# Performance work log

Hardware: AMD Instinct MI355X
Metric: run time of the kernel (lower is better)

## Reference

```python
import jax, jax.numpy as jnp
import numpy as np

IN_CH = 12
STEP = 4
UPLAG = 2048
HIDDEN = 1024
OUTPUT = 256
BATCH = 2048
FEAT = UPLAG // STEP  # per-channel conv output length


def setup_inputs() -> dict:
    key = jax.random.key(0)
    ks = jax.random.split(key, 7)
    s = 1.0 / np.sqrt(STEP)
    x = jax.random.normal(ks[0], (BATCH, IN_CH, UPLAG), dtype=jnp.float32)
    # per-channel Conv1d(1,1,step,step) weights/biases, stacked: [C, step], [C]
    W1 = jax.random.uniform(ks[1], (IN_CH, STEP), jnp.float32, -s, s)
    b1 = jax.random.uniform(ks[2], (IN_CH,), jnp.float32, -s, s)
    d_in = IN_CH * FEAT
    s2 = 1.0 / np.sqrt(d_in)
    W2 = jax.random.uniform(ks[3], (d_in, HIDDEN), jnp.float32, -s2, s2)
    b2 = jax.random.uniform(ks[4], (HIDDEN,), jnp.float32, -s2, s2)
    s3 = 1.0 / np.sqrt(HIDDEN)
    W3 = jax.random.uniform(ks[5], (HIDDEN, OUTPUT), jnp.float32, -s3, s3)
    b3 = jax.random.uniform(ks[6], (OUTPUT,), jnp.float32, -s3, s3)
    return {"x": x, "W1": W1, "b1": b1, "W2": W2, "b2": b2, "W3": W3, "b3": b3}


def reference(x, W1, b1, W2, b2, W3, b3):
    B, C, L = x.shape
    # Non-overlapping patch reduction equivalent to Conv1d(1,1,step,step) per channel:
    # view [B, C, F, step], contract step dim against per-channel kernel.
    xp = x.reshape(B, C, L // STEP, STEP)
    conv = jnp.einsum('bcfk,ck->bcf', xp, W1) + b1[None, :, None]  # [B, C, F]
    flat = conv.reshape(B, C * (L // STEP))  # concat order: channel-major, matches torch.cat
    h = jax.nn.relu(flat @ W2 + b2)
    out = h @ W3 + b3
    return out.reshape(B, 1, -1)
```

## Files before the change

kernel.cpp:

```cpp
#include <hip/hip_runtime.h>
#include <hip/hip_bf16.h>

#define BATCH   2048
#define IN_CH   12
#define UPLAG   2048
#define STEP    4
#define FEAT    512
#define DIN     6144
#define HIDDEN  1024
#define OUTPUT  256

typedef __bf16 bf16x8 __attribute__((ext_vector_type(8)));
typedef float  f32x4  __attribute__((ext_vector_type(4)));

__device__ __forceinline__ unsigned short f2bf(float f) {
  unsigned int u = __builtin_bit_cast(unsigned int, f);
  unsigned int r = (u + 0x7fffu + ((u >> 16) & 1u)) >> 16;
  return (unsigned short)r;
}

__device__ __forceinline__ void async_copy16(const unsigned short* g, unsigned short* l) {
  __builtin_amdgcn_global_load_lds(
      (const __attribute__((address_space(1))) unsigned int*)g,
      (__attribute__((address_space(3))) unsigned int*)l, 16, 0, 0);
}

__global__ __launch_bounds__(256) void conv_cast_kernel(
    const float* __restrict__ x, const float* __restrict__ W1,
    const float* __restrict__ b1, unsigned short* __restrict__ out)
{
  int gid = blockIdx.x * 256 + threadIdx.x;
  const int total = BATCH * DIN;
  if (gid >= total) return;
  int cf = gid % DIN;
  int c  = cf >> 9;
  float4 xv = ((const float4*)x)[gid];
  float4 wv = ((const float4*)W1)[c];
  float v = xv.x * wv.x + xv.y * wv.y + xv.z * wv.z + xv.w * wv.w + b1[c];
  out[gid] = f2bf(v);
}

__global__ __launch_bounds__(256) void transpose_cast(
    const float* __restrict__ in, unsigned short* __restrict__ out,
    int R, int Ncol)
{
  __shared__ float tile[32][33];
  int bx = blockIdx.x * 32;
  int by = blockIdx.y * 32;
  int tx = threadIdx.x, ty = threadIdx.y;
  #pragma unroll
  for (int i = 0; i < 32; i += 8)
    tile[ty + i][tx] = in[(size_t)(by + ty + i) * Ncol + bx + tx];
  __syncthreads();
  #pragma unroll
  for (int i = 0; i < 32; i += 8)
    out[(size_t)(bx + ty + i) * R + by + tx] = f2bf(tile[tx][ty + i]);
}

#define G1_BM 128
#define G1_BN 128
#define G1_BK 32
#define SPLITK 6

__global__ __launch_bounds__(256, 2) void gemm1_kernel(
    const unsigned short* __restrict__ A,
    const unsigned short* __restrict__ BT,
    float* __restrict__ Cp,
    int M, int N, int K)
{
  __shared__ unsigned short As[G1_BM * G1_BK];
  __shared__ unsigned short Bs[G1_BN * G1_BK];
  const int t    = threadIdx.x;
  const int lane = t & 63;
  const int wave = t >> 6;
  const int m0 = blockIdx.y * G1_BM;
  const int n0 = blockIdx.x * G1_BN;
  const int Ks = K / SPLITK;
  const int kbeg = blockIdx.z * Ks;

  const int wm = (wave >> 1) * 64;
  const int wn = (wave & 1) * 64;
  const int lm = lane & 15;
  const int lk = (lane >> 4) * 8;

  f32x4 acc[4][4];
  #pragma unroll
  for (int i = 0; i < 4; i++)
    #pragma unroll
    for (int j = 0; j < 4; j++) {
      f32x4 z = {0.f, 0.f, 0.f, 0.f};
      acc[i][j] = z;
    }

  const unsigned short* Ag = A  + (size_t)m0 * K + kbeg;
  const unsigned short* Bg = BT + (size_t)n0 * K + kbeg;

  for (int kk = 0; kk < Ks; kk += G1_BK) {
    #pragma unroll
    for (int r = 0; r < 2; ++r) {
      int chunk = r * 256 + t;
      int row = chunk >> 2;
      int kc  = (chunk & 3) * 8;
      async_copy16(Ag + (size_t)row * K + kk + kc, As + chunk * 8);
    }
    #pragma unroll
    for (int r = 0; r < 2; ++r) {
      int chunk = r * 256 + t;
      int row = chunk >> 2;
      int kc  = (chunk & 3) * 8;
      async_copy16(Bg + (size_t)row * K + kk + kc, Bs + chunk * 8);
    }
    __syncthreads();

    bf16x8 af[4], bfr[4];
    #pragma unroll
    for (int i = 0; i < 4; i++)
      af[i] = *(const bf16x8*)(As + (wm + i * 16 + lm) * G1_BK + lk);
    #pragma unroll
    for (int j = 0; j < 4; j++)
      bfr[j] = *(const bf16x8*)(Bs + (wn + j * 16 + lm) * G1_BK + lk);
    #pragma unroll
    for (int i = 0; i < 4; i++)
      #pragma unroll
      for (int j = 0; j < 4; j++)
        acc[i][j] = __builtin_amdgcn_mfma_f32_16x16x32_bf16(af[i], bfr[j], acc[i][j], 0, 0, 0);
    __syncthreads();
  }

  float* Co = Cp + (size_t)blockIdx.z * M * N;
  const int rbase = (lane >> 4) * 4;
  #pragma unroll
  for (int i = 0; i < 4; i++)
    #pragma unroll
    for (int j = 0; j < 4; j++) {
      int col = n0 + wn + j * 16 + lm;
      #pragma unroll
      for (int r = 0; r < 4; r++) {
        int row = m0 + wm + i * 16 + rbase + r;
        Co[(size_t)row * N + col] = acc[i][j][r];
      }
    }
}

__global__ __launch_bounds__(256) void reduce_bias_relu(
    const float* __restrict__ Cp, const float* __restrict__ b2,
    unsigned short* __restrict__ H)
{
  const int MN = BATCH * HIDDEN;
  int i4 = blockIdx.x * 256 + threadIdx.x;
  if (i4 >= MN / 4) return;
  float4 s = ((const float4*)Cp)[i4];
  #pragma unroll
  for (int p = 1; p < SPLITK; ++p) {
    float4 a = ((const float4*)(Cp + (size_t)p * MN))[i4];
    s.x += a.x; s.y += a.y; s.z += a.z; s.w += a.w;
  }
  int col = (i4 * 4) & (HIDDEN - 1);
  float4 bb = *(const float4*)(b2 + col);
  ushort4 o;
  o.x = f2bf(fmaxf(s.x + bb.x, 0.f));
  o.y = f2bf(fmaxf(s.y + bb.y, 0.f));
  o.z = f2bf(fmaxf(s.z + bb.z, 0.f));
  o.w = f2bf(fmaxf(s.w + bb.w, 0.f));
  ((ushort4*)H)[i4] = o;
}

#define SPLITK2 4

__global__ __launch_bounds__(256, 2) void gemm2_kernel(
    const unsigned short* __restrict__ A,
    const unsigned short* __restrict__ BT,
    float* __restrict__ Cp)
{
  const int M = BATCH, N = OUTPUT, K = HIDDEN;
  __shared__ unsigned short As[64 * 32];
  __shared__ unsigned short Bs[64 * 32];
  const int t    = threadIdx.x;
  const int lane = t & 63;
  const int wave = t >> 6;
  const int m0 = blockIdx.y * 64;
  const int n0 = blockIdx.x * 64;
  const int Ks = K / SPLITK2;
  const int kbeg = blockIdx.z * Ks;
  const int wm = (wave >> 1) * 32;
  const int wn = (wave & 1) * 32;
  const int lm = lane & 15;
  const int lk = (lane >> 4) * 8;
  const int row = t >> 2;
  const int kc  = (t & 3) * 8;

  f32x4 acc[2][2];
  #pragma unroll
  for (int i = 0; i < 2; i++)
    #pragma unroll
    for (int j = 0; j < 2; j++) {
      f32x4 z = {0.f, 0.f, 0.f, 0.f};
      acc[i][j] = z;
    }

  const unsigned short* Ag = A  + (size_t)m0 * K + kbeg;
  const unsigned short* Bg = BT + (size_t)n0 * K + kbeg;

  for (int kk = 0; kk < Ks; kk += 32) {
    async_copy16(Ag + (size_t)row * K + kk + kc, As + t * 8);
    async_copy16(Bg + (size_t)row * K + kk + kc, Bs + t * 8);
    __syncthreads();
    bf16x8 af[2], bfr[2];
    #pragma unroll
    for (int i = 0; i < 2; i++)
      af[i] = *(const bf16x8*)(As + (wm + i * 16 + lm) * 32 + lk);
    #pragma unroll
    for (int j = 0; j < 2; j++)
      bfr[j] = *(const bf16x8*)(Bs + (wn + j * 16 + lm) * 32 + lk);
    #pragma unroll
    for (int i = 0; i < 2; i++)
      #pragma unroll
      for (int j = 0; j < 2; j++)
        acc[i][j] = __builtin_amdgcn_mfma_f32_16x16x32_bf16(af[i], bfr[j], acc[i][j], 0, 0, 0);
    __syncthreads();
  }

  float* Co = Cp + (size_t)blockIdx.z * M * N;
  const int rbase = (lane >> 4) * 4;
  #pragma unroll
  for (int i = 0; i < 2; i++)
    #pragma unroll
    for (int j = 0; j < 2; j++) {
      int col = n0 + wn + j * 16 + lm;
      #pragma unroll
      for (int r = 0; r < 4; r++) {
        int row_o = m0 + wm + i * 16 + rbase + r;
        Co[(size_t)row_o * N + col] = acc[i][j][r];
      }
    }
}

__global__ __launch_bounds__(256) void reduce2_bias(
    const float* __restrict__ Cp, const float* __restrict__ b3,
    float* __restrict__ out)
{
  const int MN = BATCH * OUTPUT;
  int i4 = blockIdx.x * 256 + threadIdx.x;
  if (i4 >= MN / 4) return;
  float4 s = ((const float4*)Cp)[i4];
  #pragma unroll
  for (int p = 1; p < SPLITK2; ++p) {
    float4 a = ((const float4*)(Cp + (size_t)p * MN))[i4];
    s.x += a.x; s.y += a.y; s.z += a.z; s.w += a.w;
  }
  int col = (i4 * 4) & (OUTPUT - 1);
  float4 bb = *(const float4*)(b3 + col);
  float4 o = {s.x + bb.x, s.y + bb.y, s.z + bb.z, s.w + bb.w};
  ((float4*)out)[i4] = o;
}

extern "C" void kernel_launch(void* const* d_in, const int* in_sizes, int n_in,
                              void* d_out, int out_size, void* d_ws, size_t ws_size,
                              hipStream_t stream)
{
  const float* x  = (const float*)d_in[0];
  const float* W1 = (const float*)d_in[1];
  const float* b1 = (const float*)d_in[2];
  const float* W2 = (const float*)d_in[3];
  const float* b2 = (const float*)d_in[4];
  const float* W3 = (const float*)d_in[5];
  const float* b3 = (const float*)d_in[6];
  float* out = (float*)d_out;

  char* ws = (char*)d_ws;
  unsigned short* flatA = (unsigned short*)ws; ws += (size_t)BATCH * DIN * 2;
  unsigned short* W2T   = (unsigned short*)ws; ws += (size_t)HIDDEN * DIN * 2;
  unsigned short* W3T   = (unsigned short*)ws; ws += (size_t)OUTPUT * HIDDEN * 2;
  float*          Cpart = (float*)ws;          ws += (size_t)SPLITK * BATCH * HIDDEN * 4;
  unsigned short* H     = (unsigned short*)ws; ws += (size_t)BATCH * HIDDEN * 2;
  float*          Cp2   = (float*)ws;          ws += (size_t)SPLITK2 * BATCH * OUTPUT * 4;

  conv_cast_kernel<<<(BATCH * DIN) / 256, 256, 0, stream>>>(x, W1, b1, flatA);
  transpose_cast<<<dim3(HIDDEN / 32, DIN / 32), dim3(32, 8), 0, stream>>>(W2, W2T, DIN, HIDDEN);
  transpose_cast<<<dim3(OUTPUT / 32, HIDDEN / 32), dim3(32, 8), 0, stream>>>(W3, W3T, HIDDEN, OUTPUT);
  gemm1_kernel<<<dim3(HIDDEN / G1_BN, BATCH / G1_BM, SPLITK), 256, 0, stream>>>(
      flatA, W2T, Cpart, BATCH, HIDDEN, DIN);
  reduce_bias_relu<<<(BATCH * HIDDEN / 4) / 256, 256, 0, stream>>>(Cpart, b2, H);
  gemm2_kernel<<<dim3(OUTPUT / 64, BATCH / 64, SPLITK2), 256, 0, stream>>>(H, W3T, Cp2);
  reduce2_bias<<<(BATCH * OUTPUT / 4) / 256, 256, 0, stream>>>(Cp2, b3, out);
}
```

Measured before the change: 360.3 us.

## Store split-K partials in bf16 and remap gemm1 blocks for XCD locality

Split-K partial sums from both GEMMs are now written and read as bf16 instead of fp32, which halves the partial-buffer traffic between each GEMM and its reduction kernel. gemm1 also switches to a 1D grid whose block index is decoded so that consecutive blocks landing on the same XCD share M tiles and K slices, aiming for better L2 reuse. The cost is extra rounding error, since each partial is quantised to bf16 before summation, which could matter for accuracy tolerance.

```diff
diff --git a/kernel.cpp b/kernel.cpp
--- a/kernel.cpp
+++ b/kernel.cpp
@@ -17,6 +17,11 @@
   unsigned int u = __builtin_bit_cast(unsigned int, f);
   unsigned int r = (u + 0x7fffu + ((u >> 16) & 1u)) >> 16;
   return (unsigned short)r;
+}
+
+__device__ __forceinline__ float bf2f(unsigned short h) {
+  unsigned int u = ((unsigned int)h) << 16;
+  return __builtin_bit_cast(float, u);
 }
 
 __device__ __forceinline__ void async_copy16(const unsigned short* g, unsigned short* l) {
@@ -65,7 +70,7 @@
 __global__ __launch_bounds__(256, 2) void gemm1_kernel(
     const unsigned short* __restrict__ A,
     const unsigned short* __restrict__ BT,
-    float* __restrict__ Cp,
+    unsigned short* __restrict__ Cp,
     int M, int N, int K)
 {
   __shared__ unsigned short As[G1_BM * G1_BK];
@@ -73,10 +78,19 @@
   const int t    = threadIdx.x;
   const int lane = t & 63;
   const int wave = t >> 6;
-  const int m0 = blockIdx.y * G1_BM;
-  const int n0 = blockIdx.x * G1_BN;
+
+  int b    = blockIdx.x;
+  int xcdg = b & 7;
+  int rest = b >> 3;
+  int xt   = rest & 7;
+  int zz   = rest >> 3;
+  int zt   = zz >> 1;
+  int yt   = (xcdg << 1) | (zz & 1);
+
+  const int m0 = yt * G1_BM;
+  const int n0 = xt * G1_BN;
   const int Ks = K / SPLITK;
-  const int kbeg = blockIdx.z * Ks;
+  const int kbeg = zt * Ks;
 
   const int wm = (wave >> 1) * 64;
   const int wn = (wave & 1) * 64;
@@ -127,7 +141,7 @@
     __syncthreads();
   }
 
-  float* Co = Cp + (size_t)blockIdx.z * M * N;
+  unsigned short* Co = Cp + (size_t)zt * M * N;
   const int rbase = (lane >> 4) * 4;
   #pragma unroll
   for (int i = 0; i < 4; i++)
@@ -137,23 +151,23 @@
       #pragma unroll
       for (int r = 0; r < 4; r++) {
         int row = m0 + wm + i * 16 + rbase + r;
-        Co[(size_t)row * N + col] = acc[i][j][r];
+        Co[(size_t)row * N + col] = f2bf(acc[i][j][r]);
       }
     }
 }
 
 __global__ __launch_bounds__(256) void reduce_bias_relu(
-    const float* __restrict__ Cp, const float* __restrict__ b2,
+    const unsigned short* __restrict__ Cp, const float* __restrict__ b2,
     unsigned short* __restrict__ H)
 {
   const int MN = BATCH * HIDDEN;
   int i4 = blockIdx.x * 256 + threadIdx.x;
   if (i4 >= MN / 4) return;
-  float4 s = ((const float4*)Cp)[i4];
-  #pragma unroll
-  for (int p = 1; p < SPLITK; ++p) {
-    float4 a = ((const float4*)(Cp + (size_t)p * MN))[i4];
-    s.x += a.x; s.y += a.y; s.z += a.z; s.w += a.w;
+  float4 s = {0.f, 0.f, 0.f, 0.f};
+  #pragma unroll
+  for (int p = 0; p < SPLITK; ++p) {
+    ushort4 a = ((const ushort4*)(Cp + (size_t)p * MN))[i4];
+    s.x += bf2f(a.x); s.y += bf2f(a.y); s.z += bf2f(a.z); s.w += bf2f(a.w);
   }
   int col = (i4 * 4) & (HIDDEN - 1);
   float4 bb = *(const float4*)(b2 + col);
@@ -170,7 +184,7 @@
 __global__ __launch_bounds__(256, 2) void gemm2_kernel(
     const unsigned short* __restrict__ A,
     const unsigned short* __restrict__ BT,
-    float* __restrict__ Cp)
+    unsigned short* __restrict__ Cp)
 {
   const int M = BATCH, N = OUTPUT, K = HIDDEN;
   __shared__ unsigned short As[64 * 32];
@@ -220,7 +234,7 @@
     __syncthreads();
   }
 
-  float* Co = Cp + (size_t)blockIdx.z * M * N;
+  unsigned short* Co = Cp + (size_t)blockIdx.z * M * N;
   const int rbase = (lane >> 4) * 4;
   #pragma unroll
   for (int i = 0; i < 2; i++)
@@ -230,23 +244,23 @@
       #pragma unroll
       for (int r = 0; r < 4; r++) {
         int row_o = m0 + wm + i * 16 + rbase + r;
-        Co[(size_t)row_o * N + col] = acc[i][j][r];
+        Co[(size_t)row_o * N + col] = f2bf(acc[i][j][r]);
       }
     }
 }
 
 __global__ __launch_bounds__(256) void reduce2_bias(
-    const float* __restrict__ Cp, const float* __restrict__ b3,
+    const unsigned short* __restrict__ Cp, const float* __restrict__ b3,
     float* __restrict__ out)
 {
   const int MN = BATCH * OUTPUT;
   int i4 = blockIdx.x * 256 + threadIdx.x;
   if (i4 >= MN / 4) return;
-  float4 s = ((const float4*)Cp)[i4];
-  #pragma unroll
-  for (int p = 1; p < SPLITK2; ++p) {
-    float4 a = ((const float4*)(Cp + (size_t)p * MN))[i4];
-    s.x += a.x; s.y += a.y; s.z += a.z; s.w += a.w;
+  float4 s = {0.f, 0.f, 0.f, 0.f};
+  #pragma unroll
+  for (int p = 0; p < SPLITK2; ++p) {
+    ushort4 a = ((const ushort4*)(Cp + (size_t)p * MN))[i4];
+    s.x += bf2f(a.x); s.y += bf2f(a.y); s.z += bf2f(a.z); s.w += bf2f(a.w);
   }
   int col = (i4 * 4) & (OUTPUT - 1);
   float4 bb = *(const float4*)(b3 + col);
@@ -271,15 +285,14 @@
   unsigned short* flatA = (unsigned short*)ws; ws += (size_t)BATCH * DIN * 2;
   unsigned short* W2T   = (unsigned short*)ws; ws += (size_t)HIDDEN * DIN * 2;
   unsigned short* W3T   = (unsigned short*)ws; ws += (size_t)OUTPUT * HIDDEN * 2;
-  float*          Cpart = (float*)ws;          ws += (size_t)SPLITK * BATCH * HIDDEN * 4;
+  unsigned short* Cpart = (unsigned short*)ws; ws += (size_t)SPLITK * BATCH * HIDDEN * 2;
   unsigned short* H     = (unsigned short*)ws; ws += (size_t)BATCH * HIDDEN * 2;
-  float*          Cp2   = (float*)ws;          ws += (size_t)SPLITK2 * BATCH * OUTPUT * 4;
+  unsigned short* Cp2   = (unsigned short*)ws; ws += (size_t)SPLITK2 * BATCH * OUTPUT * 2;
 
   conv_cast_kernel<<<(BATCH * DIN) / 256, 256, 0, stream>>>(x, W1, b1, flatA);
   transpose_cast<<<dim3(HIDDEN / 32, DIN / 32), dim3(32, 8), 0, stream>>>(W2, W2T, DIN, HIDDEN);
   transpose_cast<<<dim3(OUTPUT / 32, HIDDEN / 32), dim3(32, 8), 0, stream>>>(W3, W3T, HIDDEN, OUTPUT);
-  gemm1_kernel<<<dim3(HIDDEN / G1_BN, BATCH / G1_BM, SPLITK), 256, 0, stream>>>(
-      flatA, W2T, Cpart, BATCH, HIDDEN, DIN);
+  gemm1_kernel<<<768, 256, 0, stream>>>(flatA, W2T, Cpart, BATCH, HIDDEN, DIN);
   reduce_bias_relu<<<(BATCH * HIDDEN / 4) / 256, 256, 0, stream>>>(Cpart, b2, H);
   gemm2_kernel<<<dim3(OUTPUT / 64, BATCH / 64, SPLITK2), 256, 0, stream>>>(H, W3T, Cp2);
   reduce2_bias<<<(BATCH * OUTPUT / 4) / 256, 256, 0, stream>>>(Cp2, b3, out);
```

After: 350.4 us. 1.03x faster.
